# Performance work log

Hardware: AMD Instinct MI355X
Metric: run time of the kernel (lower is better)

The kernel has to match this reference:

```python
import jax, jax.numpy as jnp
import numpy as np

N_NODES = 100000
N_EDGES = 1600000
IN_FEATS = 128
HID = 128
OUT_FEATS = 64


def setup_inputs() -> dict:
    key = jax.random.key(0)
    ks = jax.random.split(key, 8)
    node_ids = jnp.arange(N_NODES, dtype=jnp.int64)
    src = jax.random.randint(ks[0], (N_EDGES,), 0, N_NODES, dtype=jnp.int64)
    dst = jax.random.randint(ks[1], (N_EDGES,), 0, N_NODES, dtype=jnp.int64)
    emb = jax.random.normal(ks[2], (N_NODES, IN_FEATS), dtype=jnp.float32)
    W1 = jax.random.normal(ks[3], (IN_FEATS, HID), dtype=jnp.float32) / np.sqrt(IN_FEATS)
    b1 = jnp.zeros((HID,), dtype=jnp.float32)
    W2 = jax.random.normal(ks[4], (HID, OUT_FEATS), dtype=jnp.float32) / np.sqrt(HID)
    b2 = jnp.zeros((OUT_FEATS,), dtype=jnp.float32)
    return {"node_ids": node_ids, "src": src, "dst": dst, "emb": emb,
            "W1": W1, "b1": b1, "W2": W2, "b2": b2}


def _sym_norms(src, dst):
    # DGL GraphConv norm='both': D_out^{-1/2} on source side, D_in^{-1/2} on dest side,
    # degrees clamped to >= 1.
    ones = jnp.ones(src.shape[0], dtype=jnp.float32)
    deg_out = jax.ops.segment_sum(ones, src, num_segments=N_NODES)
    deg_in = jax.ops.segment_sum(ones, dst, num_segments=N_NODES)
    norm_src = jnp.clip(deg_out, 1.0, None) ** -0.5  # [N]
    norm_dst = jnp.clip(deg_in, 1.0, None) ** -0.5   # [N]
    return norm_src, norm_dst


def _spmm(src, dst, h):
    # rst[dst] += h[src]  (sparse adjacency aggregation)
    return jax.ops.segment_sum(h[src], dst, num_segments=N_NODES)


def reference(node_ids, src, dst, emb, W1, b1, W2, b2):
    norm_src, norm_dst = _sym_norms(src, dst)
    h = emb[node_ids]                                   # [N, IN]
    # Layer 1 (IN -> HID, relu): weight applied after aggregation (in <= out)
    h = _spmm(src, dst, h * norm_src[:, None]) * norm_dst[:, None]
    h = jax.nn.relu(h @ W1 + b1)                        # [N, HID]
    # Dropout(0.5) is identity in eval mode.
    # Layer 2 (HID -> OUT): DGL applies weight BEFORE aggregation when in > out
    h = (h @ W2) * norm_src[:, None]                    # [N, OUT]
    h = _spmm(src, dst, h) * norm_dst[:, None] + b2
    return h
```

## Files before the change

kernel.cpp:

```cpp
#include <hip/hip_runtime.h>

#define N_N 100000
#define N_E 1600000
#define SLOTS 48
#define N_PAD 100096

#define BK_SHIFT 8
#define BK_SIZE 256
#define NBKT 391
#define MAXB 5120
#define EPB2 2048
#define NBLK2 ((N_E + EPB2 - 1) / EPB2)
#define EPT 8

#define EMBB 6250
#define WB 96

typedef unsigned short ushort_t;
typedef unsigned int uint_t;
typedef _Float16 f16x8 __attribute__((ext_vector_type(8)));
typedef float f32x4 __attribute__((ext_vector_type(4)));

__device__ __forceinline__ ushort_t f2h(float f) {
    union { _Float16 h; ushort_t u; } c; c.h = (_Float16)f; return c.u;
}

__device__ __forceinline__ void acc2h(uint_t v, float wv, float& a, float& b) {
    union { uint_t u; _Float16 h[2]; } c; c.u = v;
    a = fmaf((float)c.h[0], wv, a);
    b = fmaf((float)c.h[1], wv, b);
}

__device__ __forceinline__ void addh(uint_t v, float& a, float& b) {
    union { uint_t u; _Float16 h[2]; } c; c.u = v;
    a += (float)c.h[0];
    b += (float)c.h[1];
}

__device__ __forceinline__ uint_t packh2(float a, float b) {
    union { _Float16 h[2]; uint_t u; } p;
    p.h[0] = (_Float16)a; p.h[1] = (_Float16)b;
    return p.u;
}

__global__ void __launch_bounds__(256) k_scatter_prep(
        const int* __restrict__ src, const int* __restrict__ dst,
        int* __restrict__ cur_d, int* __restrict__ cur_s,
        uint_t* __restrict__ pe_dst, uint_t* __restrict__ pe_src,
        const float* __restrict__ emb, ushort_t* __restrict__ embf,
        const float* __restrict__ W1, const float* __restrict__ W2,
        ushort_t* __restrict__ w1f, ushort_t* __restrict__ w2f) {
    int t = threadIdx.x, blk = blockIdx.x;
    if (blk >= NBLK2) {
        int pb = blk - NBLK2;
        if (pb < EMBB) {
            int i = pb * 512 + t;
            const float4* E4 = (const float4*)emb;
            ushort4* O4 = (ushort4*)embf;
            float4 v0 = E4[i], v1 = E4[i + 256];
            ushort4 o0, o1;
            o0.x = f2h(v0.x); o0.y = f2h(v0.y); o0.z = f2h(v0.z); o0.w = f2h(v0.w);
            o1.x = f2h(v1.x); o1.y = f2h(v1.y); o1.z = f2h(v1.z); o1.w = f2h(v1.w);
            O4[i] = o0; O4[i + 256] = o1;
        } else {
            int idx = (pb - EMBB) * 256 + t;
            int j = idx & 7, l = (idx >> 3) & 63;
            int k = (l >> 4) * 8 + j;
            int n = l & 15;
            if (idx < 16384) {
                int kc = (idx >> 9) & 3, nt = idx >> 11;
                w1f[idx] = f2h(W1[(kc * 32 + k) * 128 + nt * 16 + n]);
            } else {
                int i2 = idx - 16384;
                int kc = (i2 >> 9) & 3, nt = i2 >> 11;
                w2f[i2] = f2h(W2[(kc * 32 + k) * 64 + nt * 16 + n]);
            }
        }
        return;
    }
    __shared__ int hd[NBKT], hs[NBKT], od[NBKT], os_[NBKT];
    for (int i = t; i < NBKT; i += 256) { hd[i] = 0; hs[i] = 0; }
    __syncthreads();
    int e0 = blk * EPB2;
    int myS[EPT], myD[EPT];
    uint_t myR[EPT];
#pragma unroll
    for (int i = 0; i < EPT; i++) {
        int e = e0 + t + i * 256;
        if (e < N_E) {
            int s = src[e], d = dst[e];
            myS[i] = s; myD[i] = d;
            uint_t rd = (uint_t)atomicAdd(&hd[d >> BK_SHIFT], 1);
            uint_t rs = (uint_t)atomicAdd(&hs[s >> BK_SHIFT], 1);
            myR[i] = rd | (rs << 16);
        }
    }
    __syncthreads();
    for (int i = t; i < NBKT; i += 256) {
        int c = hd[i]; od[i]  = c ? atomicAdd(&cur_d[i], c) : 0;
        c = hs[i];     os_[i] = c ? atomicAdd(&cur_s[i], c) : 0;
    }
    __syncthreads();
#pragma unroll
    for (int i = 0; i < EPT; i++) {
        int e = e0 + t + i * 256;
        if (e < N_E) {
            int s = myS[i], d = myD[i];
            int rd = od[d >> BK_SHIFT] + (int)(myR[i] & 0xffffu);
            int rs = os_[s >> BK_SHIFT] + (int)(myR[i] >> 16);
            if (rd < MAXB) pe_dst[(size_t)(d >> BK_SHIFT) * MAXB + rd] =
                               (uint_t)s | ((uint_t)(d & 255) << 17);
            if (rs < MAXB) pe_src[(size_t)(s >> BK_SHIFT) * MAXB + rs] = (uint_t)s;
        }
    }
}

__global__ void __launch_bounds__(512) k_binC(
        const uint_t* __restrict__ pe_dst, const uint_t* __restrict__ pe_src,
        const int* __restrict__ cur_d, const int* __restrict__ cur_s,
        int* __restrict__ slots, int* __restrict__ cnt,
        float* __restrict__ nd, float* __restrict__ ns) {
    int t = threadIdx.x, bb = blockIdx.x;
    __shared__ int lc[BK_SIZE];
    __shared__ int sslot[BK_SIZE * SLOTS];
    for (int i = t; i < BK_SIZE; i += 512) lc[i] = 0;
    __syncthreads();
    if (bb < NBKT) {
        int b = bb;
        int cb = min(cur_d[b], MAXB);
        int nbase = b << BK_SHIFT;
        const uint_t* pe = pe_dst + (size_t)b * MAXB;
        for (int e = t; e < cb; e += 512) {
            uint_t ed = pe[e];
            int dloc = (int)(ed >> 17);
            int s = (int)(ed & 0x1ffffu);
            int pos = atomicAdd(&lc[dloc], 1);
            if (pos < SLOTS) sslot[dloc * SLOTS + pos] = s;
        }
        __syncthreads();
        const uint4* S4 = (const uint4*)sslot;
        uint4* G4 = (uint4*)(slots + (size_t)nbase * SLOTS);
        for (int i = t; i < BK_SIZE * SLOTS / 4; i += 512) G4[i] = S4[i];
        for (int i = t; i < BK_SIZE; i += 512) {
            int n = nbase + i;
            if (n < N_N) {
                int c = lc[i];
                cnt[n] = c;
                nd[n] = 1.0f / sqrtf((float)max(c, 1));
            }
        }
    } else {
        int b = bb - NBKT;
        int cb = min(cur_s[b], MAXB);
        int nbase = b << BK_SHIFT;
        const uint_t* pe = pe_src + (size_t)b * MAXB;
        for (int e = t; e < cb; e += 512)
            atomicAdd(&lc[(int)pe[e] - nbase], 1);
        __syncthreads();
        for (int i = t; i < BK_SIZE; i += 512) {
            int n = nbase + i;
            if (n < N_N) ns[n] = 1.0f / sqrtf((float)max(lc[i], 1));
        }
    }
}

__global__ void __launch_bounds__(256) k_spmm1(
        const int* __restrict__ cnt, const int* __restrict__ slots,
        const ushort_t* __restrict__ embf, const float* __restrict__ ns,
        const float* __restrict__ nd, uint_t* __restrict__ aggf) {
    int wid = (blockIdx.x * 256 + (int)threadIdx.x) >> 6;
    int node = __builtin_amdgcn_readfirstlane(wid);
    if (node >= N_N) return;
    int lane = threadIdx.x & 63;
    const int* row = slots + (size_t)node * SLOTS;
    int len = min(cnt[node], SLOTS);
    float ax0 = 0.f, ay0 = 0.f, ax1 = 0.f, ay1 = 0.f;
    int e = 0;
    int n8 = len & ~7;
    for (; e < n8; e += 8) {
        int s0 = __builtin_amdgcn_readfirstlane(row[e + 0]);
        int s1 = __builtin_amdgcn_readfirstlane(row[e + 1]);
        int s2 = __builtin_amdgcn_readfirstlane(row[e + 2]);
        int s3 = __builtin_amdgcn_readfirstlane(row[e + 3]);
        int s4 = __builtin_amdgcn_readfirstlane(row[e + 4]);
        int s5 = __builtin_amdgcn_readfirstlane(row[e + 5]);
        int s6 = __builtin_amdgcn_readfirstlane(row[e + 6]);
        int s7 = __builtin_amdgcn_readfirstlane(row[e + 7]);
        float w0 = ns[s0], w1 = ns[s1], w2 = ns[s2], w3 = ns[s3];
        float w4 = ns[s4], w5 = ns[s5], w6 = ns[s6], w7 = ns[s7];
        uint_t v0 = ((const uint_t*)(embf + (size_t)s0 * 128))[lane];
        uint_t v1 = ((const uint_t*)(embf + (size_t)s1 * 128))[lane];
        uint_t v2 = ((const uint_t*)(embf + (size_t)s2 * 128))[lane];
        uint_t v3 = ((const uint_t*)(embf + (size_t)s3 * 128))[lane];
        uint_t v4 = ((const uint_t*)(embf + (size_t)s4 * 128))[lane];
        uint_t v5 = ((const uint_t*)(embf + (size_t)s5 * 128))[lane];
        uint_t v6 = ((const uint_t*)(embf + (size_t)s6 * 128))[lane];
        uint_t v7 = ((const uint_t*)(embf + (size_t)s7 * 128))[lane];
        acc2h(v0, w0, ax0, ay0);
        acc2h(v1, w1, ax1, ay1);
        acc2h(v2, w2, ax0, ay0);
        acc2h(v3, w3, ax1, ay1);
        acc2h(v4, w4, ax0, ay0);
        acc2h(v5, w5, ax1, ay1);
        acc2h(v6, w6, ax0, ay0);
        acc2h(v7, w7, ax1, ay1);
    }
    int n4 = len & ~3;
    for (; e < n4; e += 4) {
        int s0 = __builtin_amdgcn_readfirstlane(row[e + 0]);
        int s1 = __builtin_amdgcn_readfirstlane(row[e + 1]);
        int s2 = __builtin_amdgcn_readfirstlane(row[e + 2]);
        int s3 = __builtin_amdgcn_readfirstlane(row[e + 3]);
        float w0 = ns[s0], w1 = ns[s1], w2 = ns[s2], w3 = ns[s3];
        uint_t v0 = ((const uint_t*)(embf + (size_t)s0 * 128))[lane];
        uint_t v1 = ((const uint_t*)(embf + (size_t)s1 * 128))[lane];
        uint_t v2 = ((const uint_t*)(embf + (size_t)s2 * 128))[lane];
        uint_t v3 = ((const uint_t*)(embf + (size_t)s3 * 128))[lane];
        acc2h(v0, w0, ax0, ay0);
        acc2h(v1, w1, ax1, ay1);
        acc2h(v2, w2, ax0, ay0);
        acc2h(v3, w3, ax1, ay1);
    }
    for (; e < len; ++e) {
        int s = __builtin_amdgcn_readfirstlane(row[e]);
        float w = ns[s];
        uint_t v = ((const uint_t*)(embf + (size_t)s * 128))[lane];
        acc2h(v, w, ax0, ay0);
    }
    float sc = nd[node];
    aggf[(size_t)node * 64 + lane] = packh2((ax0 + ax1) * sc, (ay0 + ay1) * sc);
}

#define HSTH 136
__global__ void __launch_bounds__(256) k_gemm(
        const ushort_t* __restrict__ aggf, const ushort_t* __restrict__ w1f,
        const float* __restrict__ b1, const ushort_t* __restrict__ w2f,
        const float* __restrict__ ns, ushort_t* __restrict__ h2b) {
    __shared__ ushort_t w1s[16384];
    __shared__ ushort_t w2s[8192];
    __shared__ ushort_t sh[64 * HSTH];
    int t = threadIdx.x;
    int w = t >> 6, l = t & 63;
    int quad = l >> 4, lm = l & 15;
    int nb0 = blockIdx.x * 64;

    {
        uint4* d1 = (uint4*)w1s; const uint4* g1 = (const uint4*)w1f;
        for (int i = t; i < 2048; i += 256) d1[i] = g1[i];
        uint4* d2 = (uint4*)w2s; const uint4* g2 = (const uint4*)w2f;
        for (int i = t; i < 1024; i += 256) d2[i] = g2[i];
    }

    f16x8 a[4];
#pragma unroll
    for (int kc = 0; kc < 4; kc++)
        a[kc] = *(const f16x8*)(aggf
            + (size_t)(nb0 + w * 16 + lm) * 128 + kc * 32 + quad * 8);
    __syncthreads();

    f32x4 acc[8];
#pragma unroll
    for (int nt = 0; nt < 8; nt++) acc[nt] = (f32x4){0.f, 0.f, 0.f, 0.f};
#pragma unroll
    for (int kc = 0; kc < 4; kc++) {
        f16x8 bq[8];
#pragma unroll
        for (int nt = 0; nt < 8; nt++)
            bq[nt] = *(const f16x8*)(w1s + (((nt * 4 + kc) * 64 + l) << 3));
#pragma unroll
        for (int nt = 0; nt < 8; nt++)
            acc[nt] = __builtin_amdgcn_mfma_f32_16x16x32_f16(a[kc], bq[nt], acc[nt], 0, 0, 0);
    }
#pragma unroll
    for (int nt = 0; nt < 8; nt++) {
        float bb = b1[nt * 16 + lm];
#pragma unroll
        for (int r = 0; r < 4; r++) {
            int row = w * 16 + quad * 4 + r;
            sh[row * HSTH + nt * 16 + lm] = f2h(fmaxf(acc[nt][r] + bb, 0.f));
        }
    }
    __syncthreads();

    f16x8 hh[4];
#pragma unroll
    for (int kc = 0; kc < 4; kc++)
        hh[kc] = *(const f16x8*)(sh + (w * 16 + lm) * HSTH + kc * 32 + quad * 8);

    f32x4 acc2[4];
#pragma unroll
    for (int q = 0; q < 4; q++) acc2[q] = (f32x4){0.f, 0.f, 0.f, 0.f};
#pragma unroll
    for (int kc = 0; kc < 4; kc++) {
        f16x8 b2q[4];
#pragma unroll
        for (int q = 0; q < 4; q++)
            b2q[q] = *(const f16x8*)(w2s + (((q * 4 + kc) * 64 + l) << 3));
#pragma unroll
        for (int q = 0; q < 4; q++)
            acc2[q] = __builtin_amdgcn_mfma_f32_16x16x32_f16(hh[kc], b2q[q], acc2[q], 0, 0, 0);
    }
#pragma unroll
    for (int r = 0; r < 4; r++) {
        int node = nb0 + w * 16 + quad * 4 + r;
        if (node < N_N) {
            float s = ns[node];
#pragma unroll
            for (int q = 0; q < 4; q++)
                h2b[(size_t)node * 64 + q * 16 + lm] = f2h(acc2[q][r] * s);
        }
    }
}

__global__ void __launch_bounds__(256) k_spmm2(
        const int* __restrict__ cnt, const int* __restrict__ slots,
        const ushort_t* __restrict__ h2b, const float* __restrict__ nd,
        const float* __restrict__ b2, float* __restrict__ out) {
    int wid = (blockIdx.x * 256 + (int)threadIdx.x) >> 6;
    int node = __builtin_amdgcn_readfirstlane(wid);
    if (node >= N_N) return;
    int lane = threadIdx.x & 63;
    int q = lane >> 4, w16 = lane & 15;
    const int* row = slots + (size_t)node * SLOTS;
    int len = min(cnt[node], SLOTS);
    const uint2* H2 = (const uint2*)h2b;
    float a0 = 0.f, a1 = 0.f, a2 = 0.f, a3 = 0.f;
    int e = 0;
    int n16 = len & ~15;
    for (; e < n16; e += 16) {
        const int* rp = row + e + q;
        int s0 = rp[0], s1 = rp[4], s2 = rp[8], s3 = rp[12];
        uint2 v0 = H2[(size_t)s0 * 16 + w16];
        uint2 v1 = H2[(size_t)s1 * 16 + w16];
        uint2 v2 = H2[(size_t)s2 * 16 + w16];
        uint2 v3 = H2[(size_t)s3 * 16 + w16];
        addh(v0.x, a0, a1); addh(v0.y, a2, a3);
        addh(v1.x, a0, a1); addh(v1.y, a2, a3);
        addh(v2.x, a0, a1); addh(v2.y, a2, a3);
        addh(v3.x, a0, a1); addh(v3.y, a2, a3);
    }
    int n4 = len & ~3;
    for (; e < n4; e += 4) {
        int s = row[e + q];
        uint2 v = H2[(size_t)s * 16 + w16];
        addh(v.x, a0, a1); addh(v.y, a2, a3);
    }
    if (e < len && q < len - e) {
        int s = row[e + q];
        uint2 v = H2[(size_t)s * 16 + w16];
        addh(v.x, a0, a1); addh(v.y, a2, a3);
    }
    a0 += __shfl_xor(a0, 16); a1 += __shfl_xor(a1, 16);
    a2 += __shfl_xor(a2, 16); a3 += __shfl_xor(a3, 16);
    a0 += __shfl_xor(a0, 32); a1 += __shfl_xor(a1, 32);
    a2 += __shfl_xor(a2, 32); a3 += __shfl_xor(a3, 32);
    if (q == 0) {
        float sc = nd[node];
        float4 bb = ((const float4*)b2)[w16];
        float4 o;
        o.x = a0 * sc + bb.x;
        o.y = a1 * sc + bb.y;
        o.z = a2 * sc + bb.z;
        o.w = a3 * sc + bb.w;
        ((float4*)(out + (size_t)node * 64))[w16] = o;
    }
}

extern "C" void kernel_launch(void* const* d_in, const int* in_sizes, int n_in,
                              void* d_out, int out_size, void* d_ws, size_t ws_size,
                              hipStream_t stream) {
    const int* src = (const int*)d_in[1];
    const int* dst = (const int*)d_in[2];
    const float* emb = (const float*)d_in[3];
    const float* W1 = (const float*)d_in[4];
    const float* b1 = (const float*)d_in[5];
    const float* W2 = (const float*)d_in[6];
    const float* b2 = (const float*)d_in[7];
    float* out = (float*)d_out;

    int* cur_d   = (int*)d_ws;
    int* cur_s   = cur_d + 512;
    int* cnt     = cur_s + 512;
    float* ns    = (float*)(cnt + N_PAD);
    float* nd    = ns + N_PAD;
    int* slots   = (int*)(nd + N_PAD);
    uint_t* pe_dst = (uint_t*)(slots + (size_t)N_PAD * SLOTS);
    uint_t* pe_src = pe_dst + (size_t)NBKT * MAXB;
    ushort_t* embf = (ushort_t*)(pe_src + (size_t)NBKT * MAXB);
    uint_t* aggf = (uint_t*)(embf + (size_t)N_PAD * 128);
    ushort_t* w1f = (ushort_t*)(aggf + (size_t)N_PAD * 64);
    ushort_t* w2f = w1f + 16384;
    ushort_t* h2b = w2f + 8192;

    hipMemsetAsync(cur_d, 0, sizeof(int) * 1024, stream);
    k_scatter_prep<<<NBLK2 + EMBB + WB, 256, 0, stream>>>(
        src, dst, cur_d, cur_s, pe_dst, pe_src, emb, embf, W1, W2, w1f, w2f);
    k_binC  <<<2 * NBKT, 512, 0, stream>>>(
        pe_dst, pe_src, cur_d, cur_s, slots, cnt, nd, ns);
    k_spmm1 <<<(N_N + 3) / 4, 256, 0, stream>>>(cnt, slots, embf, ns, nd, aggf);
    k_gemm  <<<N_PAD / 64, 256, 0, stream>>>((const ushort_t*)aggf, w1f, b1, w2f, ns, h2b);
    k_spmm2 <<<(N_N + 3) / 4, 256, 0, stream>>>(cnt, slots, h2b, nd, b2, out);
}
```

Measured before the change: 285.7 us.

## Stage edge bucketing in shared memory for coalesced bucket writes

The edge-binning kernel now counts bucket occupancy, prefix-sums the counts in shared memory, and scatters each edge record into a shared-memory staging buffer grouped by bucket. Each wavefront then copies whole bucket runs to global memory contiguously, replacing scattered per-edge global stores. Edges per block are doubled so each bucket run is longer. The cost is that src and dst are read twice, two block-wide scans are added, and shared-memory use grows, which may lower occupancy.

```diff
diff --git a/kernel.cpp b/kernel.cpp
--- a/kernel.cpp
+++ b/kernel.cpp
@@ -9,9 +9,9 @@
 #define BK_SIZE 256
 #define NBKT 391
 #define MAXB 5120
-#define EPB2 2048
+#define EPB2 4096
 #define NBLK2 ((N_E + EPB2 - 1) / EPB2)
-#define EPT 8
+#define EPT 16
 
 #define EMBB 6250
 #define WB 96
@@ -78,40 +78,74 @@
         }
         return;
     }
-    __shared__ int hd[NBKT], hs[NBKT], od[NBKT], os_[NBKT];
-    for (int i = t; i < NBKT; i += 256) { hd[i] = 0; hs[i] = 0; }
+    __shared__ int cntD[NBKT], cntS[NBKT], lbD[NBKT], lbS[NBKT];
+    __shared__ int gbD[NBKT], gbS[NBKT], curD[NBKT], curS[NBKT];
+    __shared__ int ps[512];
+    __shared__ uint_t recD[EPB2], recS[EPB2];
+    for (int i = t; i < NBKT; i += 256) { cntD[i] = 0; cntS[i] = 0; curD[i] = 0; curS[i] = 0; }
     __syncthreads();
     int e0 = blk * EPB2;
-    int myS[EPT], myD[EPT];
-    uint_t myR[EPT];
-#pragma unroll
+    for (int i = 0; i < EPT; i++) {
+        int e = e0 + t + i * 256;
+        if (e < N_E) {
+            atomicAdd(&cntD[dst[e] >> BK_SHIFT], 1);
+            atomicAdd(&cntS[src[e] >> BK_SHIFT], 1);
+        }
+    }
+    __syncthreads();
+    ps[t] = (t < NBKT) ? cntD[t] : 0;
+    ps[t + 256] = (t + 256 < NBKT) ? cntD[t + 256] : 0;
+    __syncthreads();
+    for (int d = 1; d < 512; d <<= 1) {
+        int v0 = (t >= d) ? ps[t - d] : 0;
+        int v1 = ps[t + 256 - d];
+        __syncthreads();
+        ps[t] += v0; ps[t + 256] += v1;
+        __syncthreads();
+    }
+    for (int b = t; b < NBKT; b += 256) {
+        int c = cntD[b];
+        lbD[b] = ps[b] - c;
+        gbD[b] = c ? atomicAdd(&cur_d[b], c) : 0;
+    }
+    __syncthreads();
+    ps[t] = (t < NBKT) ? cntS[t] : 0;
+    ps[t + 256] = (t + 256 < NBKT) ? cntS[t + 256] : 0;
+    __syncthreads();
+    for (int d = 1; d < 512; d <<= 1) {
+        int v0 = (t >= d) ? ps[t - d] : 0;
+        int v1 = ps[t + 256 - d];
+        __syncthreads();
+        ps[t] += v0; ps[t + 256] += v1;
+        __syncthreads();
+    }
+    for (int b = t; b < NBKT; b += 256) {
+        int c = cntS[b];
+        lbS[b] = ps[b] - c;
+        gbS[b] = c ? atomicAdd(&cur_s[b], c) : 0;
+    }
+    __syncthreads();
     for (int i = 0; i < EPT; i++) {
         int e = e0 + t + i * 256;
         if (e < N_E) {
             int s = src[e], d = dst[e];
-            myS[i] = s; myD[i] = d;
-            uint_t rd = (uint_t)atomicAdd(&hd[d >> BK_SHIFT], 1);
-            uint_t rs = (uint_t)atomicAdd(&hs[s >> BK_SHIFT], 1);
-            myR[i] = rd | (rs << 16);
-        }
-    }
-    __syncthreads();
-    for (int i = t; i < NBKT; i += 256) {
-        int c = hd[i]; od[i]  = c ? atomicAdd(&cur_d[i], c) : 0;
-        c = hs[i];     os_[i] = c ? atomicAdd(&cur_s[i], c) : 0;
-    }
-    __syncthreads();
-#pragma unroll
-    for (int i = 0; i < EPT; i++) {
-        int e = e0 + t + i * 256;
-        if (e < N_E) {
-            int s = myS[i], d = myD[i];
-            int rd = od[d >> BK_SHIFT] + (int)(myR[i] & 0xffffu);
-            int rs = os_[s >> BK_SHIFT] + (int)(myR[i] >> 16);
-            if (rd < MAXB) pe_dst[(size_t)(d >> BK_SHIFT) * MAXB + rd] =
-                               (uint_t)s | ((uint_t)(d & 255) << 17);
-            if (rs < MAXB) pe_src[(size_t)(s >> BK_SHIFT) * MAXB + rs] = (uint_t)s;
-        }
+            int bD = d >> BK_SHIFT;
+            int p = atomicAdd(&curD[bD], 1);
+            recD[lbD[bD] + p] = (uint_t)s | ((uint_t)(d & 255) << 17);
+            int bS = s >> BK_SHIFT;
+            int q = atomicAdd(&curS[bS], 1);
+            recS[lbS[bS] + q] = (uint_t)s;
+        }
+    }
+    __syncthreads();
+    int wv = t >> 6, ln = t & 63;
+    for (int b = wv; b < NBKT; b += 4) {
+        int c = cntD[b], lb = lbD[b], gb = gbD[b];
+        for (int j = ln; j < c; j += 64)
+            if (gb + j < MAXB) pe_dst[(size_t)b * MAXB + gb + j] = recD[lb + j];
+        c = cntS[b]; lb = lbS[b]; gb = gbS[b];
+        for (int j = ln; j < c; j += 64)
+            if (gb + j < MAXB) pe_src[(size_t)b * MAXB + gb + j] = recS[lb + j];
     }
 }
 
```

Result: slower. 308.0 us (+7.8%).

## Stage edge bucketing in shared memory for coalesced per-bucket writes

Applied to the files above, without the earlier changes.

The edge binning kernel now handles each side (dst, then src) separately. It counts edges per bucket, runs a block-wide prefix scan, scatters records into a shared-memory staging buffer grouped by bucket, and then copies each bucket's run to global memory with contiguous 16-lane writes. Edges per block double to 4096 so each bucket run is longer. This targets the scattered uncoalesced global stores of the old direct scatter, at the cost of extra LDS atomics, scan barriers, rereading src/dst, and fewer, larger blocks.

```diff
diff --git a/kernel.cpp b/kernel.cpp
--- a/kernel.cpp
+++ b/kernel.cpp
@@ -9,9 +9,9 @@
 #define BK_SIZE 256
 #define NBKT 391
 #define MAXB 5120
-#define EPB2 2048
+#define EPB2 4096
 #define NBLK2 ((N_E + EPB2 - 1) / EPB2)
-#define EPT 8
+#define EPT 16
 
 #define EMBB 6250
 #define WB 96
@@ -78,40 +78,59 @@
         }
         return;
     }
-    __shared__ int hd[NBKT], hs[NBKT], od[NBKT], os_[NBKT];
-    for (int i = t; i < NBKT; i += 256) { hd[i] = 0; hs[i] = 0; }
-    __syncthreads();
+    __shared__ int cnt_[NBKT], lb_[NBKT], gb_[NBKT], cur_[NBKT];
+    __shared__ int ps[512];
+    __shared__ uint_t rec[EPB2];
     int e0 = blk * EPB2;
-    int myS[EPT], myD[EPT];
-    uint_t myR[EPT];
-#pragma unroll
-    for (int i = 0; i < EPT; i++) {
-        int e = e0 + t + i * 256;
-        if (e < N_E) {
-            int s = src[e], d = dst[e];
-            myS[i] = s; myD[i] = d;
-            uint_t rd = (uint_t)atomicAdd(&hd[d >> BK_SHIFT], 1);
-            uint_t rs = (uint_t)atomicAdd(&hs[s >> BK_SHIFT], 1);
-            myR[i] = rd | (rs << 16);
-        }
-    }
-    __syncthreads();
-    for (int i = t; i < NBKT; i += 256) {
-        int c = hd[i]; od[i]  = c ? atomicAdd(&cur_d[i], c) : 0;
-        c = hs[i];     os_[i] = c ? atomicAdd(&cur_s[i], c) : 0;
-    }
-    __syncthreads();
-#pragma unroll
-    for (int i = 0; i < EPT; i++) {
-        int e = e0 + t + i * 256;
-        if (e < N_E) {
-            int s = myS[i], d = myD[i];
-            int rd = od[d >> BK_SHIFT] + (int)(myR[i] & 0xffffu);
-            int rs = os_[s >> BK_SHIFT] + (int)(myR[i] >> 16);
-            if (rd < MAXB) pe_dst[(size_t)(d >> BK_SHIFT) * MAXB + rd] =
-                               (uint_t)s | ((uint_t)(d & 255) << 17);
-            if (rs < MAXB) pe_src[(size_t)(s >> BK_SHIFT) * MAXB + rs] = (uint_t)s;
-        }
+    for (int side = 0; side < 2; side++) {
+        const int* key = side ? src : dst;
+        for (int i = t; i < NBKT; i += 256) { cnt_[i] = 0; cur_[i] = 0; }
+        __syncthreads();
+        for (int i = 0; i < EPT; i++) {
+            int e = e0 + t + i * 256;
+            if (e < N_E) atomicAdd(&cnt_[key[e] >> BK_SHIFT], 1);
+        }
+        __syncthreads();
+        ps[t] = (t < NBKT) ? cnt_[t] : 0;
+        ps[t + 256] = (t + 256 < NBKT) ? cnt_[t + 256] : 0;
+        __syncthreads();
+        for (int d = 1; d < 512; d <<= 1) {
+            int v0 = (t >= d) ? ps[t - d] : 0;
+            int v1 = ps[t + 256 - d];
+            __syncthreads();
+            ps[t] += v0; ps[t + 256] += v1;
+            __syncthreads();
+        }
+        int* curg = side ? cur_s : cur_d;
+        for (int b = t; b < NBKT; b += 256) {
+            int c = cnt_[b];
+            lb_[b] = ps[b] - c;
+            gb_[b] = c ? atomicAdd(&curg[b], c) : 0;
+        }
+        __syncthreads();
+        for (int i = 0; i < EPT; i++) {
+            int e = e0 + t + i * 256;
+            if (e < N_E) {
+                int s = src[e];
+                int k = side ? s : dst[e];
+                int b = k >> BK_SHIFT;
+                int p = atomicAdd(&cur_[b], 1);
+                rec[lb_[b] + p] = side ? (uint_t)s
+                                       : ((uint_t)s | ((uint_t)(k & 255) << 17));
+            }
+        }
+        __syncthreads();
+        uint_t* pe = side ? pe_src : pe_dst;
+        int wv = t >> 6, ln = t & 63, sub = ln >> 4, lj = ln & 15;
+        for (int b0 = wv * 4; b0 < NBKT; b0 += 16) {
+            int b = b0 + sub;
+            if (b < NBKT) {
+                int c = cnt_[b], lb = lb_[b], gb = gb_[b];
+                for (int j = lj; j < c; j += 16)
+                    if (gb + j < MAXB) pe[(size_t)b * MAXB + gb + j] = rec[lb + j];
+            }
+        }
+        __syncthreads();
     }
 }
 
```

Measured after the change: 285.1 us, median of 2. No clear change (-0.2%).
